# Performance work log

Hardware: AMD Instinct MI355X
Metric: run time of the kernel (lower is better)

## Reference

```python
import jax, jax.numpy as jnp
import numpy as np

D, DFF, H = 768, 3072, 12
HD = D // H
EPS = 1e-12

def _ln(t, gamma, beta):
    mu = t.mean(-1, keepdims=True)
    var = jnp.mean((t - mu) ** 2, -1, keepdims=True)
    return gamma * (t - mu) / jnp.sqrt(var + EPS) + beta

def setup_inputs() -> dict:
    key = jax.random.key(0)
    ks = jax.random.split(key, 16)
    s = 0.02
    x = jax.random.normal(ks[0], (2, 2048, D), jnp.float32)
    mask = jnp.ones((2, 2048), jnp.float32)
    def lin(k, out_d, in_d):
        kw, kb = jax.random.split(k)
        return (jax.random.normal(kw, (out_d, in_d), jnp.float32) * s,
                jnp.zeros((out_d,), jnp.float32))
    Wq, bq = lin(ks[1], D, D)
    Wk, bk = lin(ks[2], D, D)
    Wv, bv = lin(ks[3], D, D)
    Wp, bp = lin(ks[4], D, D)
    W1, bf1 = lin(ks[5], DFF, D)
    W2, bf2 = lin(ks[6], D, DFF)
    g1 = jnp.ones((D,), jnp.float32); be1 = jnp.zeros((D,), jnp.float32)
    g2 = jnp.ones((D,), jnp.float32); be2 = jnp.zeros((D,), jnp.float32)
    return dict(x=x, mask=mask, Wq=Wq, bq=bq, Wk=Wk, bk=bk, Wv=Wv, bv=bv,
                Wp=Wp, bp=bp, g1=g1, be1=be1, W1=W1, bf1=bf1, W2=W2, bf2=bf2,
                g2=g2, be2=be2)

def reference(x, mask, Wq, bq, Wk, bk, Wv, bv, Wp, bp, g1, be1, W1, bf1, W2, bf2, g2, be2):
    B, S, _ = x.shape
    # projections (torch Linear: x @ W^T + b)
    q = (x @ Wq.T + bq).reshape(B, S, H, HD).transpose(0, 2, 1, 3)  # [B,H,S,HD]
    k = (x @ Wk.T + bk).reshape(B, S, H, HD).transpose(0, 2, 1, 3)
    v = (x @ Wv.T + bv).reshape(B, S, H, HD).transpose(0, 2, 1, 3)
    scores = jnp.einsum('bhqd,bhkd->bhqk', q, k) / jnp.sqrt(jnp.float32(HD))
    scores = scores - 10000.0 * (1.0 - mask[:, None, None, :])
    p = jax.nn.softmax(scores, axis=-1)  # dropout is identity at eval
    h = jnp.einsum('bhqk,bhkd->bqhd', p, v).reshape(B, S, D)
    h = h @ Wp.T + bp
    x1 = _ln(x + h, g1, be1)
    ff = jax.nn.gelu(x1 @ W1.T + bf1, approximate=False) @ W2.T + bf2
    return _ln(x1 + ff, g2, be2)
```

## Files before the change

kernel.cpp:

```cpp
#include <hip/hip_runtime.h>
#include <hip/hip_bf16.h>
#include <math.h>

#define D_MODEL 768
#define D_FF    3072
#define N_HEAD  12
#define HEAD_D  64
#define BATCH   2
#define SEQ     2048
#define QKV_LD  2304

typedef __attribute__((ext_vector_type(8))) short short8;
typedef __attribute__((ext_vector_type(8))) unsigned short ushort8;
typedef __attribute__((ext_vector_type(4))) float f32x4;

__device__ inline unsigned short f2bf(float f) {
    union { __hip_bfloat16 b; unsigned short u; } cv;
    cv.b = __float2bfloat16(f);
    return cv.u;
}

__device__ inline float bf2f(unsigned short u) {
    union { unsigned int i; float f; } cv;
    cv.i = ((unsigned int)u) << 16;
    return cv.f;
}

__device__ inline void async_load16(const void* g, void* l) {
    __builtin_amdgcn_global_load_lds(
        (const __attribute__((address_space(1))) void*)g,
        (__attribute__((address_space(3))) void*)l, 16, 0, 0);
}

__global__ __launch_bounds__(256) void conv_fused(
    const float* __restrict__ x,
    const float* __restrict__ Wq, const float* __restrict__ Wk,
    const float* __restrict__ Wv, const float* __restrict__ Wp,
    const float* __restrict__ W1, const float* __restrict__ W2,
    const float* __restrict__ bq, const float* __restrict__ bk,
    const float* __restrict__ bv,
    unsigned short* __restrict__ xb, unsigned short* __restrict__ wqkvb,
    unsigned short* __restrict__ wpb, unsigned short* __restrict__ w1b,
    unsigned short* __restrict__ w2b, float* __restrict__ bqkv)
{
    int bid = blockIdx.x;
    const float* src; unsigned short* dst; int base;
    if      (bid < 3072) { src = x;  dst = xb;              base = bid;        }
    else if (bid < 3648) { src = Wq; dst = wqkvb;           base = bid - 3072; }
    else if (bid < 4224) { src = Wk; dst = wqkvb + 589824;  base = bid - 3648; }
    else if (bid < 4800) { src = Wv; dst = wqkvb + 1179648; base = bid - 4224; }
    else if (bid < 5376) { src = Wp; dst = wpb;             base = bid - 4800; }
    else if (bid < 7680) { src = W1; dst = w1b;             base = bid - 5376; }
    else if (bid < 9984) { src = W2; dst = w2b;             base = bid - 7680; }
    else {
        for (int j = threadIdx.x; j < QKV_LD; j += 256)
            bqkv[j] = (j < 768) ? bq[j] : (j < 1536) ? bk[j - 768] : bv[j - 1536];
        return;
    }
    int i = (base * 256 + threadIdx.x) * 4;
    float4 v = *(const float4*)(src + i);
    ushort4 o4;
    o4.x = f2bf(v.x); o4.y = f2bf(v.y); o4.z = f2bf(v.z); o4.w = f2bf(v.w);
    *(ushort4*)(dst + i) = o4;
}

#define NSTAGE 3

__global__ __launch_bounds__(256) void gemm_bf16(
    const unsigned short* __restrict__ A, int lda,
    const unsigned short* __restrict__ W, int ldw,
    const float* __restrict__ bias,
    const unsigned short* __restrict__ resb, int ldr,
    float* __restrict__ outf, unsigned short* __restrict__ outb,
    float* __restrict__ pacc, int ldo,
    int M, int N, int K, int mode)
{
    __shared__ unsigned short As[NSTAGE][128 * 32];
    __shared__ unsigned short Bs[NSTAGE][128 * 32];

    const int t    = threadIdx.x;
    const int lane = t & 63;
    const int wv   = t >> 6;
    const int wm   = wv >> 1;
    const int wn   = wv & 1;
    const int bm   = blockIdx.y * 128;
    const int bn   = blockIdx.x * 128;
    const int kz   = blockIdx.z;
    const int Kc   = K / gridDim.z;

    const int qd   = lane >> 4;
    const int l16  = lane & 15;

    f32x4 acc[4][4];
    #pragma unroll
    for (int i = 0; i < 4; i++)
        #pragma unroll
        for (int j = 0; j < 4; j++)
            acc[i][j] = (f32x4){0.f, 0.f, 0.f, 0.f};

    const int srow = lane >> 2;
    const int sseg = (lane & 3) * 8;
    const int r0   = (wv * 2 + 0) * 16 + srow;
    const int r1   = (wv * 2 + 1) * 16 + srow;
    const size_t gA0 = (size_t)(bm + r0) * lda + sseg;
    const size_t gA1 = (size_t)(bm + r1) * lda + sseg;
    const size_t gB0 = (size_t)(bn + r0) * ldw + sseg;
    const size_t gB1 = (size_t)(bn + r1) * ldw + sseg;
    const int c0 = (wv * 2 + 0) * 512;
    const int c1 = (wv * 2 + 1) * 512;

    const int kbeg  = kz * Kc;
    const int niter = Kc / 32;

    async_load16(A + gA0 + kbeg, &As[0][c0]);
    async_load16(W + gB0 + kbeg, &Bs[0][c0]);
    async_load16(A + gA1 + kbeg, &As[0][c1]);
    async_load16(W + gB1 + kbeg, &Bs[0][c1]);
    if (niter > 1) {
        async_load16(A + gA0 + kbeg + 32, &As[1][c0]);
        async_load16(W + gB0 + kbeg + 32, &Bs[1][c0]);
        async_load16(A + gA1 + kbeg + 32, &As[1][c1]);
        async_load16(W + gB1 + kbeg + 32, &Bs[1][c1]);
    }

    int stage = 0;
    for (int it = 0; it < niter; it++) {
        if (it + 1 < niter) __builtin_amdgcn_s_waitcnt(0x0F74);
        else                __builtin_amdgcn_s_waitcnt(0x0F70);
        __builtin_amdgcn_s_barrier();

        if (it + 2 < niter) {
            const int sn = (stage + 2 >= NSTAGE) ? stage + 2 - NSTAGE : stage + 2;
            const int kn = kbeg + (it + 2) * 32;
            async_load16(A + gA0 + kn, &As[sn][c0]);
            async_load16(W + gB0 + kn, &Bs[sn][c0]);
            async_load16(A + gA1 + kn, &As[sn][c1]);
            async_load16(W + gB1 + kn, &Bs[sn][c1]);
        }

        short8 af[4], bf[4];
        #pragma unroll
        for (int mt = 0; mt < 4; mt++)
            af[mt] = *(const short8*)(&As[stage][(wm * 64 + mt * 16 + l16) * 32 + qd * 8]);
        #pragma unroll
        for (int nt = 0; nt < 4; nt++)
            bf[nt] = *(const short8*)(&Bs[stage][(wn * 64 + nt * 16 + l16) * 32 + qd * 8]);
        #pragma unroll
        for (int mt = 0; mt < 4; mt++)
            #pragma unroll
            for (int nt = 0; nt < 4; nt++)
                acc[mt][nt] = __builtin_amdgcn_mfma_f32_16x16x32_bf16(
                    af[mt], bf[nt], acc[mt][nt], 0, 0, 0);

        stage = (stage == NSTAGE - 1) ? 0 : stage + 1;
    }

    #pragma unroll
    for (int mt = 0; mt < 4; mt++) {
        #pragma unroll
        for (int nt = 0; nt < 4; nt++) {
            int col = bn + wn * 64 + nt * 16 + l16;
            float bv = (kz == 0) ? bias[col] : 0.f;
            #pragma unroll
            for (int r = 0; r < 4; r++) {
                int row = bm + wm * 64 + mt * 16 + qd * 4 + r;
                if (kz != 0) {
                    pacc[(size_t)row * ldo + col] = acc[mt][nt][r];
                    continue;
                }
                float v = acc[mt][nt][r] + bv;
                if (mode == 1) {
                    v += bf2f(resb[(size_t)row * ldr + col]);
                    outf[(size_t)row * ldo + col] = v;
                } else if (mode == 2) {
                    v = 0.5f * v * (1.0f + erff(v * 0.70710678118654752f));
                    outb[(size_t)row * ldo + col] = f2bf(v);
                } else if (mode == 3) {
                    outb[(size_t)row * ldo + col] = f2bf(v);
                } else {
                    outf[(size_t)row * ldo + col] = v;
                }
            }
        }
    }
}

__global__ __launch_bounds__(256) void gemm_qkv(
    const unsigned short* __restrict__ A,
    const unsigned short* __restrict__ W,
    const float* __restrict__ bias,
    unsigned short* __restrict__ outb)
{
    __shared__ unsigned short As[4][128 * 32];
    __shared__ unsigned short Bs[4][128 * 32];

    const int t    = threadIdx.x;
    const int lane = t & 63;
    const int wv   = t >> 6;
    const int wm   = wv >> 1;
    const int wn   = wv & 1;

    const int flat = blockIdx.y * 18 + blockIdx.x;
    const int xcd  = flat & 7;
    const int u    = flat >> 3;
    const int mi   = (xcd >> 1) * 8 + u / 9;
    const int ni   = (xcd & 1) * 9 + u % 9;
    const int bm   = mi * 128;
    const int bn   = ni * 128;

    const int qd   = lane >> 4;
    const int l16  = lane & 15;

    f32x4 acc[4][4];
    #pragma unroll
    for (int i = 0; i < 4; i++)
        #pragma unroll
        for (int j = 0; j < 4; j++)
            acc[i][j] = (f32x4){0.f, 0.f, 0.f, 0.f};

    const int srow = lane >> 2;
    const int sseg = (lane & 3) * 8;
    const int r0   = (wv * 2 + 0) * 16 + srow;
    const int r1   = (wv * 2 + 1) * 16 + srow;
    const size_t gA0 = (size_t)(bm + r0) * D_MODEL + sseg;
    const size_t gA1 = (size_t)(bm + r1) * D_MODEL + sseg;
    const size_t gB0 = (size_t)(bn + r0) * D_MODEL + sseg;
    const size_t gB1 = (size_t)(bn + r1) * D_MODEL + sseg;
    const int c0 = (wv * 2 + 0) * 512;
    const int c1 = (wv * 2 + 1) * 512;

    const int niter = D_MODEL / 32;

    async_load16(A + gA0, &As[0][c0]);
    async_load16(W + gB0, &Bs[0][c0]);
    async_load16(A + gA1, &As[0][c1]);
    async_load16(W + gB1, &Bs[0][c1]);
    async_load16(A + gA0 + 32, &As[1][c0]);
    async_load16(W + gB0 + 32, &Bs[1][c0]);
    async_load16(A + gA1 + 32, &As[1][c1]);
    async_load16(W + gB1 + 32, &Bs[1][c1]);
    async_load16(A + gA0 + 64, &As[2][c0]);
    async_load16(W + gB0 + 64, &Bs[2][c0]);
    async_load16(A + gA1 + 64, &As[2][c1]);
    async_load16(W + gB1 + 64, &Bs[2][c1]);

    int stage = 0;
    for (int it = 0; it < niter; it++) {
        if      (it + 2 < niter) __builtin_amdgcn_s_waitcnt(0x0F78);
        else if (it + 1 < niter) __builtin_amdgcn_s_waitcnt(0x0F74);
        else                     __builtin_amdgcn_s_waitcnt(0x0F70);
        __builtin_amdgcn_s_barrier();

        if (it + 3 < niter) {
            int sn = stage + 3;
            if (sn >= 4) sn -= 4;
            const int kn = (it + 3) * 32;
            async_load16(A + gA0 + kn, &As[sn][c0]);
            async_load16(W + gB0 + kn, &Bs[sn][c0]);
            async_load16(A + gA1 + kn, &As[sn][c1]);
            async_load16(W + gB1 + kn, &Bs[sn][c1]);
        }

        short8 af[4], bf[4];
        #pragma unroll
        for (int mt = 0; mt < 4; mt++)
            af[mt] = *(const short8*)(&As[stage][(wm * 64 + mt * 16 + l16) * 32 + qd * 8]);
        #pragma unroll
        for (int nt = 0; nt < 4; nt++)
            bf[nt] = *(const short8*)(&Bs[stage][(wn * 64 + nt * 16 + l16) * 32 + qd * 8]);
        #pragma unroll
        for (int mt = 0; mt < 4; mt++)
            #pragma unroll
            for (int nt = 0; nt < 4; nt++)
                acc[mt][nt] = __builtin_amdgcn_mfma_f32_16x16x32_bf16(
                    af[mt], bf[nt], acc[mt][nt], 0, 0, 0);

        stage = (stage == 3) ? 0 : stage + 1;
    }

    #pragma unroll
    for (int mt = 0; mt < 4; mt++) {
        #pragma unroll
        for (int nt = 0; nt < 4; nt++) {
            int col = bn + wn * 64 + nt * 16 + l16;
            float bv = bias[col];
            #pragma unroll
            for (int r = 0; r < 4; r++) {
                int row = bm + wm * 64 + mt * 16 + qd * 4 + r;
                outb[(size_t)row * QKV_LD + col] = f2bf(acc[mt][nt][r] + bv);
            }
        }
    }
}

__global__ __launch_bounds__(256) void gemm_ffn1(
    const unsigned short* __restrict__ A,
    const unsigned short* __restrict__ W,
    const float* __restrict__ bias,
    unsigned short* __restrict__ outb)
{
    __shared__ unsigned short As[NSTAGE][128 * 32];
    __shared__ unsigned short Bs[NSTAGE][128 * 32];

    const int t    = threadIdx.x;
    const int lane = t & 63;
    const int wv   = t >> 6;
    const int wm   = wv >> 1;
    const int wn   = wv & 1;

    const int flat = blockIdx.y * 24 + blockIdx.x;
    const int xcd  = flat & 7;
    const int u    = flat >> 3;
    const int mi   = (xcd >> 1) * 8 + u / 12;
    const int ni   = (xcd & 1) * 12 + u % 12;
    const int bm   = mi * 128;
    const int bn   = ni * 128;

    const int qd   = lane >> 4;
    const int l16  = lane & 15;

    f32x4 acc[4][4];
    #pragma unroll
    for (int i = 0; i < 4; i++)
        #pragma unroll
        for (int j = 0; j < 4; j++)
            acc[i][j] = (f32x4){0.f, 0.f, 0.f, 0.f};

    const int srow = lane >> 2;
    const int sseg = (lane & 3) * 8;
    const int r0   = (wv * 2 + 0) * 16 + srow;
    const int r1   = (wv * 2 + 1) * 16 + srow;
    const size_t gA0 = (size_t)(bm + r0) * D_MODEL + sseg;
    const size_t gA1 = (size_t)(bm + r1) * D_MODEL + sseg;
    const size_t gB0 = (size_t)(bn + r0) * D_MODEL + sseg;
    const size_t gB1 = (size_t)(bn + r1) * D_MODEL + sseg;
    const int c0 = (wv * 2 + 0) * 512;
    const int c1 = (wv * 2 + 1) * 512;

    const int niter = D_MODEL / 32;

    async_load16(A + gA0, &As[0][c0]);
    async_load16(W + gB0, &Bs[0][c0]);
    async_load16(A + gA1, &As[0][c1]);
    async_load16(W + gB1, &Bs[0][c1]);
    async_load16(A + gA0 + 32, &As[1][c0]);
    async_load16(W + gB0 + 32, &Bs[1][c0]);
    async_load16(A + gA1 + 32, &As[1][c1]);
    async_load16(W + gB1 + 32, &Bs[1][c1]);

    int stage = 0;
    for (int it = 0; it < niter; it++) {
        if (it + 1 < niter) __builtin_amdgcn_s_waitcnt(0x0F74);
        else                __builtin_amdgcn_s_waitcnt(0x0F70);
        __builtin_amdgcn_s_barrier();

        if (it + 2 < niter) {
            const int sn = (stage + 2 >= NSTAGE) ? stage + 2 - NSTAGE : stage + 2;
            const int kn = (it + 2) * 32;
            async_load16(A + gA0 + kn, &As[sn][c0]);
            async_load16(W + gB0 + kn, &Bs[sn][c0]);
            async_load16(A + gA1 + kn, &As[sn][c1]);
            async_load16(W + gB1 + kn, &Bs[sn][c1]);
        }

        short8 af[4], bf[4];
        #pragma unroll
        for (int mt = 0; mt < 4; mt++)
            af[mt] = *(const short8*)(&As[stage][(wm * 64 + mt * 16 + l16) * 32 + qd * 8]);
        #pragma unroll
        for (int nt = 0; nt < 4; nt++)
            bf[nt] = *(const short8*)(&Bs[stage][(wn * 64 + nt * 16 + l16) * 32 + qd * 8]);
        #pragma unroll
        for (int mt = 0; mt < 4; mt++)
            #pragma unroll
            for (int nt = 0; nt < 4; nt++)
                acc[mt][nt] = __builtin_amdgcn_mfma_f32_16x16x32_bf16(
                    af[mt], bf[nt], acc[mt][nt], 0, 0, 0);

        stage = (stage == NSTAGE - 1) ? 0 : stage + 1;
    }

    #pragma unroll
    for (int mt = 0; mt < 4; mt++) {
        #pragma unroll
        for (int nt = 0; nt < 4; nt++) {
            int col = bn + wn * 64 + nt * 16 + l16;
            float bv = bias[col];
            #pragma unroll
            for (int r = 0; r < 4; r++) {
                int row = bm + wm * 64 + mt * 16 + qd * 4 + r;
                float v = acc[mt][nt][r] + bv;
                v = 0.5f * v * (1.0f + erff(v * 0.70710678118654752f));
                outb[(size_t)row * D_FF + col] = f2bf(v);
            }
        }
    }
}

__global__ __launch_bounds__(256) void gemm_ffn2(
    const unsigned short* __restrict__ A,
    const unsigned short* __restrict__ W,
    const float* __restrict__ bias,
    const unsigned short* __restrict__ resb,
    float* __restrict__ outf,
    float* __restrict__ pacc)
{
    __shared__ unsigned short As[NSTAGE][128 * 32];
    __shared__ unsigned short Bs[NSTAGE][128 * 32];

    const int t    = threadIdx.x;
    const int lane = t & 63;
    const int wv   = t >> 6;
    const int wm   = wv >> 1;
    const int wn   = wv & 1;

    const int flat = blockIdx.x;
    const int g    = flat & 7;
    const int u    = flat >> 3;
    const int kz   = g >> 2;
    const int g2   = g & 3;
    const int band = u / 24;
    const int rr   = (u % 24) / 6;
    const int cc   = u % 6;
    const int bm   = (g2 * 8 + band * 4 + rr) * 128;
    const int bn   = cc * 128;

    const int qd   = lane >> 4;
    const int l16  = lane & 15;

    f32x4 acc[4][4];
    #pragma unroll
    for (int i = 0; i < 4; i++)
        #pragma unroll
        for (int j = 0; j < 4; j++)
            acc[i][j] = (f32x4){0.f, 0.f, 0.f, 0.f};

    const int srow = lane >> 2;
    const int sseg = (lane & 3) * 8;
    const int r0   = (wv * 2 + 0) * 16 + srow;
    const int r1   = (wv * 2 + 1) * 16 + srow;
    const size_t gA0 = (size_t)(bm + r0) * D_FF + sseg;
    const size_t gA1 = (size_t)(bm + r1) * D_FF + sseg;
    const size_t gB0 = (size_t)(bn + r0) * D_FF + sseg;
    const size_t gB1 = (size_t)(bn + r1) * D_FF + sseg;
    const int c0 = (wv * 2 + 0) * 512;
    const int c1 = (wv * 2 + 1) * 512;

    const int kbeg  = kz * (D_FF / 2);
    const int niter = (D_FF / 2) / 32;

    async_load16(A + gA0 + kbeg, &As[0][c0]);
    async_load16(W + gB0 + kbeg, &Bs[0][c0]);
    async_load16(A + gA1 + kbeg, &As[0][c1]);
    async_load16(W + gB1 + kbeg, &Bs[0][c1]);
    async_load16(A + gA0 + kbeg + 32, &As[1][c0]);
    async_load16(W + gB0 + kbeg + 32, &Bs[1][c0]);
    async_load16(A + gA1 + kbeg + 32, &As[1][c1]);
    async_load16(W + gB1 + kbeg + 32, &Bs[1][c1]);

    int stage = 0;
    for (int it = 0; it < niter; it++) {
        if (it + 1 < niter) __builtin_amdgcn_s_waitcnt(0x0F74);
        else                __builtin_amdgcn_s_waitcnt(0x0F70);
        __builtin_amdgcn_s_barrier();

        if (it + 2 < niter) {
            const int sn = (stage + 2 >= NSTAGE) ? stage + 2 - NSTAGE : stage + 2;
            const int kn = kbeg + (it + 2) * 32;
            async_load16(A + gA0 + kn, &As[sn][c0]);
            async_load16(W + gB0 + kn, &Bs[sn][c0]);
            async_load16(A + gA1 + kn, &As[sn][c1]);
            async_load16(W + gB1 + kn, &Bs[sn][c1]);
        }

        short8 af[4], bf[4];
        #pragma unroll
        for (int mt = 0; mt < 4; mt++)
            af[mt] = *(const short8*)(&As[stage][(wm * 64 + mt * 16 + l16) * 32 + qd * 8]);
        #pragma unroll
        for (int nt = 0; nt < 4; nt++)
            bf[nt] = *(const short8*)(&Bs[stage][(wn * 64 + nt * 16 + l16) * 32 + qd * 8]);
        #pragma unroll
        for (int mt = 0; mt < 4; mt++)
            #pragma unroll
            for (int nt = 0; nt < 4; nt++)
                acc[mt][nt] = __builtin_amdgcn_mfma_f32_16x16x32_bf16(
                    af[mt], bf[nt], acc[mt][nt], 0, 0, 0);

        stage = (stage == NSTAGE - 1) ? 0 : stage + 1;
    }

    #pragma unroll
    for (int mt = 0; mt < 4; mt++) {
        #pragma unroll
        for (int nt = 0; nt < 4; nt++) {
            int col = bn + wn * 64 + nt * 16 + l16;
            #pragma unroll
            for (int r = 0; r < 4; r++) {
                int row = bm + wm * 64 + mt * 16 + qd * 4 + r;
                if (kz != 0) {
                    pacc[(size_t)row * D_MODEL + col] = acc[mt][nt][r];
                } else {
                    float v = acc[mt][nt][r] + bias[col]
                            + bf2f(resb[(size_t)row * D_MODEL + col]);
                    outf[(size_t)row * D_MODEL + col] = v;
                }
            }
        }
    }
}

__global__ __launch_bounds__(256) void vtrans(
    const unsigned short* __restrict__ qkv, unsigned short* __restrict__ vT)
{
    __shared__ unsigned short T[64 * 72];
    const int t   = threadIdx.x;
    const int kt  = blockIdx.x;
    const int bh  = blockIdx.y;
    const int h   = bh % N_HEAD;
    const int b   = bh / N_HEAD;
    const int row = t >> 2;
    const int c0  = (t & 3) * 16;

    const unsigned short* src =
        qkv + (size_t)(b * SEQ + kt * 64 + row) * QKV_LD + 1536 + h * HEAD_D + c0;
    *(ushort8*)&T[row * 72 + c0]     = *(const ushort8*)src;
    *(ushort8*)&T[row * 72 + c0 + 8] = *(const ushort8*)(src + 8);
    __syncthreads();

    const int d = t >> 2;
    ushort8 o0, o1;
    #pragma unroll
    for (int j = 0; j < 8; j++) o0[j] = T[(c0 + j) * 72 + d];
    #pragma unroll
    for (int j = 0; j < 8; j++) o1[j] = T[(c0 + 8 + j) * 72 + d];
    unsigned short* dst = vT + ((size_t)bh * HEAD_D + d) * SEQ + kt * 64 + c0;
    *(ushort8*)dst       = o0;
    *(ushort8*)(dst + 8) = o1;
}

#define ASTR 72
#define VSTR 136

__global__ __launch_bounds__(256) void attn_mfma(
    const unsigned short* __restrict__ qkv, const unsigned short* __restrict__ vT,
    const float* __restrict__ mask, unsigned short* __restrict__ out)
{
    __shared__ __align__(16) unsigned short Ks[128 * ASTR];
    __shared__ __align__(16) unsigned short Vt[64 * VSTR];
    __shared__ float Ms[128];

    const int t    = threadIdx.x;
    const int lane = t & 63;
    const int wv   = t >> 6;
    const int l16  = lane & 15;
    const int quad = lane >> 4;
    const int q0   = blockIdx.x * 64;
    const int bh   = blockIdx.y;
    const int h    = bh % N_HEAD;
    const int b    = bh / N_HEAD;
    const int NT   = SEQ / 128;

    const unsigned short* qb  = qkv + (size_t)b * SEQ * QKV_LD + h * HEAD_D;
    const unsigned short* kb  = qb + 768;
    const unsigned short* vtb = vT + (size_t)bh * HEAD_D * SEQ;

    {
        const int qsrow = t >> 2;
        const int qsc0  = (t & 3) * 16;
        const ushort8* src = (const ushort8*)(qb + (size_t)(q0 + qsrow) * QKV_LD + qsc0);
        *(ushort8*)&Ks[qsrow * ASTR + qsc0]     = src[0];
        *(ushort8*)&Ks[qsrow * ASTR + qsc0 + 8] = src[1];
    }
    __syncthreads();
    short8 bq0 = *(const short8*)&Ks[(wv * 16 + l16) * ASTR + quad * 8];
    short8 bq1 = *(const short8*)&Ks[(wv * 16 + l16) * ASTR + 32 + quad * 8];
    __syncthreads();

    const int krow_s = t >> 1;
    const int kc0    = (t & 1) * 32;
    const int ks6    = krow_s & 63;
    const int ksig   = (krow_s & 64) |
                       ((ks6 & 0x23) | ((ks6 & 0x04) << 2) | ((ks6 & 0x18) >> 1));
    const int vrow_s = t >> 2;
    const int vc0    = (t & 3) * 32;

    f32x4 o[4];
    #pragma unroll
    for (int i = 0; i < 4; i++) o[i] = (f32x4){0.f, 0.f, 0.f, 0.f};
    float m_st = -INFINITY, l_st = 0.f;

    ushort8 rk0, rk1, rk2, rk3, rv0, rv1, rv2, rv3;
    float rm = 1.0f;
    {
        const ushort8* ksrc = (const ushort8*)(kb + (size_t)krow_s * QKV_LD + kc0);
        rk0 = ksrc[0]; rk1 = ksrc[1]; rk2 = ksrc[2]; rk3 = ksrc[3];
        const ushort8* vsrc = (const ushort8*)(vtb + (size_t)vrow_s * SEQ + vc0);
        rv0 = vsrc[0]; rv1 = vsrc[1]; rv2 = vsrc[2]; rv3 = vsrc[3];
        if (t < 128) rm = mask[b * SEQ + t];
    }

    for (int kt = 0; kt < NT; kt++) {
        *(ushort8*)&Ks[ksig * ASTR + kc0]      = rk0;
        *(ushort8*)&Ks[ksig * ASTR + kc0 + 8]  = rk1;
        *(ushort8*)&Ks[ksig * ASTR + kc0 + 16] = rk2;
        *(ushort8*)&Ks[ksig * ASTR + kc0 + 24] = rk3;
        *(ushort8*)&Vt[vrow_s * VSTR + vc0]      = rv0;
        *(ushort8*)&Vt[vrow_s * VSTR + vc0 + 8]  = rv1;
        *(ushort8*)&Vt[vrow_s * VSTR + vc0 + 16] = rv2;
        *(ushort8*)&Vt[vrow_s * VSTR + vc0 + 24] = rv3;
        if (t < 128) Ms[t] = -10000.0f * (1.0f - rm);
        __syncthreads();

        if (kt + 1 < NT) {
            const int kn = (kt + 1) * 128;
            const ushort8* ksrc = (const ushort8*)(kb + (size_t)(kn + krow_s) * QKV_LD + kc0);
            rk0 = ksrc[0]; rk1 = ksrc[1]; rk2 = ksrc[2]; rk3 = ksrc[3];
            const ushort8* vsrc = (const ushort8*)(vtb + (size_t)vrow_s * SEQ + kn + vc0);
            rv0 = vsrc[0]; rv1 = vsrc[1]; rv2 = vsrc[2]; rv3 = vsrc[3];
            if (t < 128) rm = mask[b * SEQ + kn + t];
        }

        float p[8][4];
        float mx = -3.0e38f;
        #pragma unroll
        for (int bi = 0; bi < 8; bi++) {
            const int krow = (bi * 16 + l16) * ASTR;
            short8 k0 = *(const short8*)&Ks[krow + quad * 8];
            short8 k1 = *(const short8*)&Ks[krow + 32 + quad * 8];
            f32x4 z = (f32x4){0.f, 0.f, 0.f, 0.f};
            z = __builtin_amdgcn_mfma_f32_16x16x32_bf16(k0, bq0, z, 0, 0, 0);
            z = __builtin_amdgcn_mfma_f32_16x16x32_bf16(k1, bq1, z, 0, 0, 0);
            const float4 m4 = *(const float4*)
                &Ms[(bi >> 2) * 64 + ((bi >> 1) & 1) * 32 + quad * 8 + (bi & 1) * 4];
            #pragma unroll
            for (int r = 0; r < 4; r++) {
                float s = fmaf(z[r], 0.125f, ((const float*)&m4)[r]);
                p[bi][r] = s;
                mx = fmaxf(mx, s);
            }
        }
        mx = fmaxf(mx, __shfl_xor(mx, 16, 64));
        mx = fmaxf(mx, __shfl_xor(mx, 32, 64));
        float m_new = fmaxf(m_st, mx);
        float alpha = __expf(m_st - m_new);
        m_st = m_new;
        float ls = 0.f;
        #pragma unroll
        for (int bi = 0; bi < 8; bi++) {
            #pragma unroll
            for (int r = 0; r < 4; r++) {
                p[bi][r] = __expf(p[bi][r] - m_new);
                ls += p[bi][r];
            }
        }
        ls += __shfl_xor(ls, 16, 64);
        ls += __shfl_xor(ls, 32, 64);
        l_st = l_st * alpha + ls;

        float ar[4];
        #pragma unroll
        for (int r = 0; r < 4; r++) ar[r] = __shfl(alpha, quad * 4 + r, 64);
        #pragma unroll
        for (int nt = 0; nt < 4; nt++)
            #pragma unroll
            for (int r = 0; r < 4; r++)
                o[nt][r] *= ar[r];

        short8 pf[4];
        #pragma unroll
        for (int w = 0; w < 4; w++) {
            #pragma unroll
            for (int bsel = 0; bsel < 2; bsel++) {
                #pragma unroll
                for (int r = 0; r < 4; r++)
                    pf[w][bsel * 4 + r] = (short)f2bf(p[w * 2 + bsel][r]);
            }
        }

        #pragma unroll
        for (int nt = 0; nt < 4; nt++) {
            const int vrow = (nt * 16 + l16) * VSTR;
            #pragma unroll
            for (int w = 0; w < 4; w++) {
                short8 vv = *(const short8*)&Vt[vrow + w * 32 + quad * 8];
                o[nt] = __builtin_amdgcn_mfma_f32_16x16x32_bf16(pf[w], vv, o[nt], 0, 0, 0);
            }
        }
        __syncthreads();
    }

    float inv = 1.0f / l_st;
    float ir[4];
    #pragma unroll
    for (int r = 0; r < 4; r++) ir[r] = __shfl(inv, quad * 4 + r, 64);
    #pragma unroll
    for (int nt = 0; nt < 4; nt++) {
        #pragma unroll
        for (int r = 0; r < 4; r++) {
            int qi = q0 + wv * 16 + quad * 4 + r;
            out[(size_t)(b * SEQ + qi) * D_MODEL + h * HEAD_D + nt * 16 + l16] =
                f2bf(o[nt][r] * ir[r]);
        }
    }
}

__global__ __launch_bounds__(256) void ln_kernel(
    const float* __restrict__ in, const float* __restrict__ in2,
    const float* __restrict__ g, const float* __restrict__ be,
    float* __restrict__ outf, unsigned short* __restrict__ outb)
{
    const int row = blockIdx.x;
    const int t   = threadIdx.x;
    const float* rp  = in  + (size_t)row * D_MODEL;
    const float* rp2 = in2 ? in2 + (size_t)row * D_MODEL : nullptr;

    float vals[3];
    float s = 0.f, s2 = 0.f;
    #pragma unroll
    for (int i = 0; i < 3; i++) {
        float x = rp[t + i * 256];
        if (rp2) x += rp2[t + i * 256];
        vals[i] = x;
        s += x; s2 += x * x;
    }
    #pragma unroll
    for (int off = 32; off >= 1; off >>= 1) {
        s  += __shfl_xor(s,  off, 64);
        s2 += __shfl_xor(s2, off, 64);
    }
    __shared__ float rs[4], rs2[4];
    __shared__ float mu_s, rstd_s;
    const int wave = t >> 6, lane = t & 63;
    if (lane == 0) { rs[wave] = s; rs2[wave] = s2; }
    __syncthreads();
    if (t == 0) {
        float S1 = rs[0] + rs[1] + rs[2] + rs[3];
        float S2 = rs2[0] + rs2[1] + rs2[2] + rs2[3];
        float mu  = S1 * (1.0f / D_MODEL);
        float var = S2 * (1.0f / D_MODEL) - mu * mu;
        mu_s = mu;
        rstd_s = rsqrtf(var + 1e-12f);
    }
    __syncthreads();
    const float mu = mu_s, rstd = rstd_s;
    #pragma unroll
    for (int i = 0; i < 3; i++) {
        int c = t + i * 256;
        float o = g[c] * (vals[i] - mu) * rstd + be[c];
        if (outf) outf[(size_t)row * D_MODEL + c] = o;
        if (outb) outb[(size_t)row * D_MODEL + c] = f2bf(o);
    }
}

extern "C" void kernel_launch(void* const* d_in, const int* in_sizes, int n_in,
                              void* d_out, int out_size, void* d_ws, size_t ws_size,
                              hipStream_t stream)
{
    const float* x    = (const float*)d_in[0];
    const float* mask = (const float*)d_in[1];
    const float* Wq   = (const float*)d_in[2];
    const float* bq   = (const float*)d_in[3];
    const float* Wk   = (const float*)d_in[4];
    const float* bk   = (const float*)d_in[5];
    const float* Wv   = (const float*)d_in[6];
    const float* bv   = (const float*)d_in[7];
    const float* Wp   = (const float*)d_in[8];
    const float* bp   = (const float*)d_in[9];
    const float* g1   = (const float*)d_in[10];
    const float* be1  = (const float*)d_in[11];
    const float* W1   = (const float*)d_in[12];
    const float* bf1  = (const float*)d_in[13];
    const float* W2   = (const float*)d_in[14];
    const float* bf2  = (const float*)d_in[15];
    const float* g2   = (const float*)d_in[16];
    const float* be2  = (const float*)d_in[17];

    const int M = BATCH * SEQ;

    char* ws = (char*)d_ws;
    unsigned short* qkvb  = (unsigned short*)(ws + 0);
    unsigned short* ff1b  = (unsigned short*)(ws + 0);
    unsigned short* xb    = (unsigned short*)(ws + 25165824);
    unsigned short* hb    = (unsigned short*)(ws + 31457280);
    unsigned short* x1b   = (unsigned short*)(ws + 31457280);
    float*          y0    = (float*)(ws + 37748736);
    unsigned short* wqkvb = (unsigned short*)(ws + 50331648);
    unsigned short* wpb   = (unsigned short*)(ws + 53870592);
    unsigned short* w1b   = (unsigned short*)(ws + 55050240);
    unsigned short* w2b   = (unsigned short*)(ws + 59768832);
    float*          bqkv  = (float*)(ws + 64487424);
    float*          p1    = (float*)(ws + 64496640);
    unsigned short* vTb   = (unsigned short*)(ws + 77079552);

    dim3 blk(256);

    conv_fused<<<dim3(9985), blk, 0, stream>>>(
        x, Wq, Wk, Wv, Wp, W1, W2, bq, bk, bv,
        xb, wqkvb, wpb, w1b, w2b, bqkv);

    gemm_qkv<<<dim3(QKV_LD / 128, M / 128), blk, 0, stream>>>(xb, wqkvb, bqkv, qkvb);

    vtrans<<<dim3(SEQ / 64, BATCH * N_HEAD), blk, 0, stream>>>(qkvb, vTb);

    attn_mfma<<<dim3(SEQ / 64, BATCH * N_HEAD), blk, 0, stream>>>(qkvb, vTb, mask, hb);

    gemm_bf16<<<dim3(D_MODEL / 128, M / 128, 2), blk, 0, stream>>>(
        hb, D_MODEL, wpb, D_MODEL, bp, xb, D_MODEL,
        y0, nullptr, p1, D_MODEL, M, D_MODEL, D_MODEL, 1);

    ln_kernel<<<dim3(M), blk, 0, stream>>>(y0, p1, g1, be1, nullptr, x1b);

    gemm_ffn1<<<dim3(D_FF / 128, M / 128), blk, 0, stream>>>(x1b, w1b, bf1, ff1b);

    gemm_ffn2<<<dim3(384), blk, 0, stream>>>(ff1b, w2b, bf2, x1b, y0, p1);

    ln_kernel<<<dim3(M), blk, 0, stream>>>(y0, p1, g2, be2, (float*)d_out, nullptr);
}
```

Baseline: 345.9 us.

## Use BK=64 double-buffered tiles with XOR-swizzled LDS in FFN2 GEMM

Rewrites the FFN2 GEMM main loop to load 64-wide K tiles into two LDS buffers instead of 32-wide tiles in a multi-stage ring. The LDS layout uses an XOR swizzle on the 16-byte column slot to avoid bank conflicts on fragment reads. This halves the number of barriers per K and issues more MFMAs per iteration. The trade-off is a shallower prefetch depth, since the code now waits for all outstanding loads each iteration, which may expose more global-load latency.

Result: faster. 336.0 us (-2.9%).

```diff
diff --git a/kernel.cpp b/kernel.cpp
--- a/kernel.cpp
+++ b/kernel.cpp
@@ -405,8 +405,8 @@
     float* __restrict__ outf,
     float* __restrict__ pacc)
 {
-    __shared__ unsigned short As[NSTAGE][128 * 32];
-    __shared__ unsigned short Bs[NSTAGE][128 * 32];
+    __shared__ unsigned short As[2][128 * 64];
+    __shared__ unsigned short Bs[2][128 * 64];
 
     const int t    = threadIdx.x;
     const int lane = t & 63;
@@ -435,59 +435,57 @@
         for (int j = 0; j < 4; j++)
             acc[i][j] = (f32x4){0.f, 0.f, 0.f, 0.f};
 
-    const int srow = lane >> 2;
-    const int sseg = (lane & 3) * 8;
-    const int r0   = (wv * 2 + 0) * 16 + srow;
-    const int r1   = (wv * 2 + 1) * 16 + srow;
-    const size_t gA0 = (size_t)(bm + r0) * D_FF + sseg;
-    const size_t gA1 = (size_t)(bm + r1) * D_FF + sseg;
-    const size_t gB0 = (size_t)(bn + r0) * D_FF + sseg;
-    const size_t gB1 = (size_t)(bn + r1) * D_FF + sseg;
-    const int c0 = (wv * 2 + 0) * 512;
-    const int c1 = (wv * 2 + 1) * 512;
+    const int srow8 = lane >> 3;
+    const int scol  = ((lane & 7) ^ srow8) * 8;
+    const size_t gA_base = (size_t)(bm + wv * 32 + srow8) * D_FF + scol;
+    const size_t gB_base = (size_t)(bn + wv * 32 + srow8) * D_FF + scol;
+    const int ldsb = wv * 4 * 512;
 
     const int kbeg  = kz * (D_FF / 2);
-    const int niter = (D_FF / 2) / 32;
-
-    async_load16(A + gA0 + kbeg, &As[0][c0]);
-    async_load16(W + gB0 + kbeg, &Bs[0][c0]);
-    async_load16(A + gA1 + kbeg, &As[0][c1]);
-    async_load16(W + gB1 + kbeg, &Bs[0][c1]);
-    async_load16(A + gA0 + kbeg + 32, &As[1][c0]);
-    async_load16(W + gB0 + kbeg + 32, &Bs[1][c0]);
-    async_load16(A + gA1 + kbeg + 32, &As[1][c1]);
-    async_load16(W + gB1 + kbeg + 32, &Bs[1][c1]);
-
-    int stage = 0;
+    const int niter = (D_FF / 2) / 64;
+
+    #pragma unroll
+    for (int j = 0; j < 4; j++) {
+        async_load16(A + gA_base + (size_t)(j * 8) * D_FF + kbeg, &As[0][ldsb + j * 512]);
+        async_load16(W + gB_base + (size_t)(j * 8) * D_FF + kbeg, &Bs[0][ldsb + j * 512]);
+    }
+
     for (int it = 0; it < niter; it++) {
-        if (it + 1 < niter) __builtin_amdgcn_s_waitcnt(0x0F74);
-        else                __builtin_amdgcn_s_waitcnt(0x0F70);
+        __builtin_amdgcn_s_waitcnt(0x0F70);
         __builtin_amdgcn_s_barrier();
-
-        if (it + 2 < niter) {
-            const int sn = (stage + 2 >= NSTAGE) ? stage + 2 - NSTAGE : stage + 2;
-            const int kn = kbeg + (it + 2) * 32;
-            async_load16(A + gA0 + kn, &As[sn][c0]);
-            async_load16(W + gB0 + kn, &Bs[sn][c0]);
-            async_load16(A + gA1 + kn, &As[sn][c1]);
-            async_load16(W + gB1 + kn, &Bs[sn][c1]);
-        }
-
-        short8 af[4], bf[4];
-        #pragma unroll
-        for (int mt = 0; mt < 4; mt++)
-            af[mt] = *(const short8*)(&As[stage][(wm * 64 + mt * 16 + l16) * 32 + qd * 8]);
-        #pragma unroll
-        for (int nt = 0; nt < 4; nt++)
-            bf[nt] = *(const short8*)(&Bs[stage][(wn * 64 + nt * 16 + l16) * 32 + qd * 8]);
-        #pragma unroll
-        for (int mt = 0; mt < 4; mt++)
-            #pragma unroll
-            for (int nt = 0; nt < 4; nt++)
-                acc[mt][nt] = __builtin_amdgcn_mfma_f32_16x16x32_bf16(
-                    af[mt], bf[nt], acc[mt][nt], 0, 0, 0);
-
-        stage = (stage == NSTAGE - 1) ? 0 : stage + 1;
+        const int st = it & 1;
+
+        if (it + 1 < niter) {
+            const int kn = kbeg + (it + 1) * 64;
+            #pragma unroll
+            for (int j = 0; j < 4; j++) {
+                async_load16(A + gA_base + (size_t)(j * 8) * D_FF + kn, &As[st ^ 1][ldsb + j * 512]);
+                async_load16(W + gB_base + (size_t)(j * 8) * D_FF + kn, &Bs[st ^ 1][ldsb + j * 512]);
+            }
+        }
+
+        #pragma unroll
+        for (int kk = 0; kk < 2; kk++) {
+            short8 af[4], bf[4];
+            #pragma unroll
+            for (int mt = 0; mt < 4; mt++) {
+                const int row = wm * 64 + mt * 16 + l16;
+                const int slot = (kk * 4 + qd) ^ (row & 7);
+                af[mt] = *(const short8*)&As[st][row * 64 + slot * 8];
+            }
+            #pragma unroll
+            for (int nt = 0; nt < 4; nt++) {
+                const int row = wn * 64 + nt * 16 + l16;
+                const int slot = (kk * 4 + qd) ^ (row & 7);
+                bf[nt] = *(const short8*)&Bs[st][row * 64 + slot * 8];
+            }
+            #pragma unroll
+            for (int mt = 0; mt < 4; mt++)
+                #pragma unroll
+                for (int nt = 0; nt < 4; nt++)
+                    acc[mt][nt] = __builtin_amdgcn_mfma_f32_16x16x32_bf16(
+                        af[mt], bf[nt], acc[mt][nt], 0, 0, 0);
+        }
     }
 
     #pragma unroll
```
